# Kernel tuning notes

Measured on AMD Instinct MI355X. Metric: run time of the kernel, lower is better.

Reference implementation:

```python
import jax, jax.numpy as jnp
import numpy as np

DIM = 4096
CAP = 8192
EPS = 1e-8  # torch F.cosine_similarity denominator clamp


def setup_inputs() -> dict:
    key = jax.random.key(0)
    k1, k2, k3, k4, k5, k6 = jax.random.split(key, 6)
    return {
        "query": jax.random.normal(k1, (DIM,), dtype=jnp.float32),
        "memory_bank": jax.random.normal(k2, (CAP, DIM), dtype=jnp.float32),
        "importance": jax.random.uniform(k3, (CAP,), dtype=jnp.float32),
        "age": jax.random.uniform(k4, (CAP,), dtype=jnp.float32) * 1000.0,
        "W_dec": jax.random.normal(k5, (DIM, DIM), dtype=jnp.float32) * (1.0 / np.sqrt(DIM)),
        "b_dec": jax.random.normal(k6, (DIM,), dtype=jnp.float32) * 0.01,
        "top_k": 8,
    }


def reference(query, memory_bank, importance, age, W_dec, b_dec, top_k):
    # Cosine similarity of query against every memory row (torch semantics:
    # dot / max(||q||*||m||, eps)).
    dots = memory_bank @ query                       # [CAP]
    qn = jnp.sqrt(jnp.sum(query * query))
    mn = jnp.sqrt(jnp.sum(memory_bank * memory_bank, axis=1))
    sim = dots / jnp.maximum(qn * mn, EPS)
    # Time-decayed importance weighting.
    weighted = sim * importance * jnp.exp(-0.001 * age)
    # Top-k retrieval, mean-pool retrieved rows, decode.
    _, idx = jax.lax.top_k(weighted, top_k)          # [k]
    retrieved = jnp.mean(memory_bank[idx], axis=0)   # [DIM]
    return retrieved @ W_dec.T + b_dec
```

## Files before the change

### kernel.cpp

```cpp
#include <hip/hip_runtime.h>
#include <math.h>

#define DIM 4096
#define CAP 8192
#define EPS 1e-8f

__global__ __launch_bounds__(256) void score_kernel(
    const float* __restrict__ q,
    const float* __restrict__ mb,
    const float* __restrict__ imp,
    const float* __restrict__ age,
    float* __restrict__ weighted)
{
    const int wave = threadIdx.x >> 6;
    const int lane = threadIdx.x & 63;
    const int row  = (blockIdx.x << 2) + wave;

    const float4* __restrict__ mrow = (const float4*)(mb + (size_t)row * DIM);
    const float4* __restrict__ q4   = (const float4*)q;

    float dot = 0.f, msq = 0.f, qsq = 0.f;
    #pragma unroll 4
    for (int i = lane; i < DIM / 4; i += 64) {
        float4 m  = mrow[i];
        float4 qq = q4[i];
        dot = fmaf(m.w, qq.w, fmaf(m.z, qq.z, fmaf(m.y, qq.y, fmaf(m.x, qq.x, dot))));
        msq = fmaf(m.w, m.w,  fmaf(m.z, m.z,  fmaf(m.y, m.y,  fmaf(m.x, m.x,  msq))));
        qsq = fmaf(qq.w, qq.w, fmaf(qq.z, qq.z, fmaf(qq.y, qq.y, fmaf(qq.x, qq.x, qsq))));
    }
    #pragma unroll
    for (int off = 32; off > 0; off >>= 1) {
        dot += __shfl_down(dot, off, 64);
        msq += __shfl_down(msq, off, 64);
        qsq += __shfl_down(qsq, off, 64);
    }
    if (lane == 0) {
        float denom = fmaxf(sqrtf(qsq) * sqrtf(msq), EPS);
        weighted[row] = (dot / denom) * imp[row] * expf(-0.001f * age[row]);
    }
}

__global__ __launch_bounds__(256) void topk_decode_kernel(
    const float* __restrict__ weighted,
    const float* __restrict__ mb,
    const int* __restrict__ topk_ptr,
    const float* __restrict__ W,
    const float* __restrict__ b,
    float* __restrict__ out)
{
    __shared__ float rbar[DIM];
    __shared__ float rv[4];
    __shared__ int   ri[4];
    __shared__ int   sidx[64];

    const int tid  = threadIdx.x;
    const int wave = tid >> 6;
    const int lane = tid & 63;

    int k = *topk_ptr;
    if (k < 1) k = 1;
    if (k > 64) k = 64;

    const float4* __restrict__ w4 = (const float4*)weighted;
    float4 val[8];
    #pragma unroll
    for (int j = 0; j < 8; ++j) val[j] = w4[(j << 8) + tid];

    float bv = -INFINITY; int bi = 0x7fffffff;
    #pragma unroll
    for (int j = 0; j < 8; ++j) {
        const int base = (j << 10) + (tid << 2);
        if (val[j].x > bv) { bv = val[j].x; bi = base + 0; }
        if (val[j].y > bv) { bv = val[j].y; bi = base + 1; }
        if (val[j].z > bv) { bv = val[j].z; bi = base + 2; }
        if (val[j].w > bv) { bv = val[j].w; bi = base + 3; }
    }

    for (int it = 0; it < k; ++it) {
        float cv = bv; int ci = bi;
        #pragma unroll
        for (int off = 32; off > 0; off >>= 1) {
            float ov = __shfl_down(cv, off, 64);
            int   oi = __shfl_down(ci, off, 64);
            if (ov > cv || (ov == cv && oi < ci)) { cv = ov; ci = oi; }
        }
        if (lane == 0) { rv[wave] = cv; ri[wave] = ci; }
        __syncthreads();
        if (tid == 0) {
            float best = rv[0]; int besti = ri[0];
            #pragma unroll
            for (int w = 1; w < 4; ++w) {
                if (rv[w] > best || (rv[w] == best && ri[w] < besti)) {
                    best = rv[w]; besti = ri[w];
                }
            }
            sidx[it] = besti;
        }
        __syncthreads();
        const int gbi = sidx[it];
        if (((gbi >> 2) & 255) == tid) {
            const int jr = gbi >> 10;
            const int cr = gbi & 3;
            #pragma unroll
            for (int j = 0; j < 8; ++j) {
                if (j == jr) {
                    if (cr == 0) val[j].x = -INFINITY;
                    if (cr == 1) val[j].y = -INFINITY;
                    if (cr == 2) val[j].z = -INFINITY;
                    if (cr == 3) val[j].w = -INFINITY;
                }
            }
            bv = -INFINITY; bi = 0x7fffffff;
            #pragma unroll
            for (int j = 0; j < 8; ++j) {
                const int base = (j << 10) + (tid << 2);
                if (val[j].x > bv) { bv = val[j].x; bi = base + 0; }
                if (val[j].y > bv) { bv = val[j].y; bi = base + 1; }
                if (val[j].z > bv) { bv = val[j].z; bi = base + 2; }
                if (val[j].w > bv) { bv = val[j].w; bi = base + 3; }
            }
        }
    }
    __syncthreads();

    const float inv_k = 1.0f / (float)k;
    float4* __restrict__ rbar4 = (float4*)rbar;
    for (int i = tid; i < DIM / 4; i += 256) {
        float4 acc = make_float4(0.f, 0.f, 0.f, 0.f);
        for (int r = 0; r < k; ++r) {
            const float4 v = ((const float4*)(mb + (size_t)sidx[r] * DIM))[i];
            acc.x += v.x; acc.y += v.y; acc.z += v.z; acc.w += v.w;
        }
        acc.x *= inv_k; acc.y *= inv_k; acc.z *= inv_k; acc.w *= inv_k;
        rbar4[i] = acc;
    }
    __syncthreads();

    const int j = (blockIdx.x << 2) + wave;
    const float4* __restrict__ wrow = (const float4*)(W + (size_t)j * DIM);

    float acc = 0.f;
    #pragma unroll 4
    for (int i = lane; i < DIM / 4; i += 64) {
        float4 w = wrow[i];
        float4 v = rbar4[i];
        acc = fmaf(w.w, v.w, fmaf(w.z, v.z, fmaf(w.y, v.y, fmaf(w.x, v.x, acc))));
    }
    #pragma unroll
    for (int off = 32; off > 0; off >>= 1) acc += __shfl_down(acc, off, 64);
    if (lane == 0) out[j] = acc + b[j];
}

extern "C" void kernel_launch(void* const* d_in, const int* in_sizes, int n_in,
                              void* d_out, int out_size, void* d_ws, size_t ws_size,
                              hipStream_t stream) {
    const float* query      = (const float*)d_in[0];
    const float* memory     = (const float*)d_in[1];
    const float* importance = (const float*)d_in[2];
    const float* age        = (const float*)d_in[3];
    const float* W_dec      = (const float*)d_in[4];
    const float* b_dec      = (const float*)d_in[5];
    const int*   top_k      = (const int*)d_in[6];

    float* weighted = (float*)d_ws;
    float* out      = (float*)d_out;

    score_kernel<<<CAP / 4, 256, 0, stream>>>(query, memory, importance, age, weighted);
    topk_decode_kernel<<<DIM / 4, 256, 0, stream>>>(weighted, memory, top_k,
                                                    W_dec, b_dec, out);
}
```

Before: 254.7 us.

## Make top-k selection wave-local with LDS scores and prefetch W row early

Each wave now runs the full top-k selection on its own, from a copy of all weighted scores staged in shared memory. Selected entries are tracked with per-lane bitmasks, and the lane that owned a winner rescans its candidates. This removes the two block-wide barriers per top-k iteration. The W_dec row is loaded into registers before the selection starts so its global latency overlaps the serial selection, and the gather of the mean-pooled row is split across waves. In exchange, every wave repeats the selection work, and the 64 float4 registers of W plus the 48KB of shared memory per block may reduce occupancy.

```diff
diff --git a/kernel.cpp b/kernel.cpp
--- a/kernel.cpp
+++ b/kernel.cpp
@@ -48,10 +48,9 @@
     const float* __restrict__ b,
     float* __restrict__ out)
 {
+    __shared__ float wv[CAP];
     __shared__ float rbar[DIM];
-    __shared__ float rv[4];
-    __shared__ int   ri[4];
-    __shared__ int   sidx[64];
+    __shared__ int   sidx[4][64];
 
     const int tid  = threadIdx.x;
     const int wave = tid >> 6;
@@ -61,89 +60,85 @@
     if (k < 1) k = 1;
     if (k > 64) k = 64;
 
-    const float4* __restrict__ w4 = (const float4*)weighted;
-    float4 val[8];
+    {
+        const float4* __restrict__ w4  = (const float4*)weighted;
+        float4* __restrict__       wv4 = (float4*)wv;
+        #pragma unroll
+        for (int i = tid; i < CAP / 4; i += 256) wv4[i] = w4[i];
+    }
+    __syncthreads();
+
+    const int j = (blockIdx.x << 2) + wave;
+    const float4* __restrict__ wrow4 = (const float4*)(W + (size_t)j * DIM);
+    float4 wreg[16];
     #pragma unroll
-    for (int j = 0; j < 8; ++j) val[j] = w4[(j << 8) + tid];
+    for (int t = 0; t < 16; ++t) wreg[t] = wrow4[lane + (t << 6)];
 
-    float bv = -INFINITY; int bi = 0x7fffffff;
-    #pragma unroll
-    for (int j = 0; j < 8; ++j) {
-        const int base = (j << 10) + (tid << 2);
-        if (val[j].x > bv) { bv = val[j].x; bi = base + 0; }
-        if (val[j].y > bv) { bv = val[j].y; bi = base + 1; }
-        if (val[j].z > bv) { bv = val[j].z; bi = base + 2; }
-        if (val[j].w > bv) { bv = val[j].w; bi = base + 3; }
-    }
+    const float4* __restrict__ wv4 = (const float4*)wv;
+    unsigned long long cons0 = 0ULL, cons1 = 0ULL;
+
+    float bv; int bi;
+    auto rescan = [&]() {
+        bv = -INFINITY; bi = 0x7fffffff;
+        #pragma unroll
+        for (int t = 0; t < 32; ++t) {
+            const float4 v = wv4[lane + (t << 6)];
+            const int base = (lane << 2) + (t << 8);
+            const unsigned long long m = (t < 16) ? cons0 : cons1;
+            const int sh = (t & 15) << 2;
+            if (!((m >> (sh + 0)) & 1ULL) && v.x > bv) { bv = v.x; bi = base + 0; }
+            if (!((m >> (sh + 1)) & 1ULL) && v.y > bv) { bv = v.y; bi = base + 1; }
+            if (!((m >> (sh + 2)) & 1ULL) && v.z > bv) { bv = v.z; bi = base + 2; }
+            if (!((m >> (sh + 3)) & 1ULL) && v.w > bv) { bv = v.w; bi = base + 3; }
+        }
+    };
+    rescan();
 
     for (int it = 0; it < k; ++it) {
         float cv = bv; int ci = bi;
         #pragma unroll
         for (int off = 32; off > 0; off >>= 1) {
-            float ov = __shfl_down(cv, off, 64);
-            int   oi = __shfl_down(ci, off, 64);
+            float ov = __shfl_xor(cv, off, 64);
+            int   oi = __shfl_xor(ci, off, 64);
             if (ov > cv || (ov == cv && oi < ci)) { cv = ov; ci = oi; }
         }
-        if (lane == 0) { rv[wave] = cv; ri[wave] = ci; }
-        __syncthreads();
-        if (tid == 0) {
-            float best = rv[0]; int besti = ri[0];
-            #pragma unroll
-            for (int w = 1; w < 4; ++w) {
-                if (rv[w] > best || (rv[w] == best && ri[w] < besti)) {
-                    best = rv[w]; besti = ri[w];
-                }
-            }
-            sidx[it] = besti;
+        if (lane == 0) sidx[wave][it] = ci;
+        if (((ci >> 2) & 63) == lane) {
+            const int jp = ((ci >> 8) << 2) | (ci & 3);
+            if (jp < 64) cons0 |= 1ULL << jp;
+            else         cons1 |= 1ULL << (jp - 64);
+            rescan();
         }
-        __syncthreads();
-        const int gbi = sidx[it];
-        if (((gbi >> 2) & 255) == tid) {
-            const int jr = gbi >> 10;
-            const int cr = gbi & 3;
-            #pragma unroll
-            for (int j = 0; j < 8; ++j) {
-                if (j == jr) {
-                    if (cr == 0) val[j].x = -INFINITY;
-                    if (cr == 1) val[j].y = -INFINITY;
-                    if (cr == 2) val[j].z = -INFINITY;
-                    if (cr == 3) val[j].w = -INFINITY;
-                }
-            }
-            bv = -INFINITY; bi = 0x7fffffff;
-            #pragma unroll
-            for (int j = 0; j < 8; ++j) {
-                const int base = (j << 10) + (tid << 2);
-                if (val[j].x > bv) { bv = val[j].x; bi = base + 0; }
-                if (val[j].y > bv) { bv = val[j].y; bi = base + 1; }
-                if (val[j].z > bv) { bv = val[j].z; bi = base + 2; }
-                if (val[j].w > bv) { bv = val[j].w; bi = base + 3; }
-            }
+    }
+    __builtin_amdgcn_wave_barrier();
+
+    float4 racc[4];
+    #pragma unroll
+    for (int t = 0; t < 4; ++t) racc[t] = make_float4(0.f, 0.f, 0.f, 0.f);
+    for (int r = 0; r < k; ++r) {
+        const int idx = sidx[wave][r];
+        const float4* __restrict__ mrow4 = (const float4*)(mb + (size_t)idx * DIM);
+        #pragma unroll
+        for (int t = 0; t < 4; ++t) {
+            const float4 v = mrow4[(wave << 8) + (t << 6) + lane];
+            racc[t].x += v.x; racc[t].y += v.y; racc[t].z += v.z; racc[t].w += v.w;
         }
+    }
+    const float inv_k = 1.0f / (float)k;
+    float4* __restrict__ rbar4 = (float4*)rbar;
+    #pragma unroll
+    for (int t = 0; t < 4; ++t) {
+        racc[t].x *= inv_k; racc[t].y *= inv_k;
+        racc[t].z *= inv_k; racc[t].w *= inv_k;
+        rbar4[(wave << 8) + (t << 6) + lane] = racc[t];
     }
     __syncthreads();
 
-    const float inv_k = 1.0f / (float)k;
-    float4* __restrict__ rbar4 = (float4*)rbar;
-    for (int i = tid; i < DIM / 4; i += 256) {
-        float4 acc = make_float4(0.f, 0.f, 0.f, 0.f);
-        for (int r = 0; r < k; ++r) {
-            const float4 v = ((const float4*)(mb + (size_t)sidx[r] * DIM))[i];
-            acc.x += v.x; acc.y += v.y; acc.z += v.z; acc.w += v.w;
-        }
-        acc.x *= inv_k; acc.y *= inv_k; acc.z *= inv_k; acc.w *= inv_k;
-        rbar4[i] = acc;
-    }
-    __syncthreads();
-
-    const int j = (blockIdx.x << 2) + wave;
-    const float4* __restrict__ wrow = (const float4*)(W + (size_t)j * DIM);
-
     float acc = 0.f;
-    #pragma unroll 4
-    for (int i = lane; i < DIM / 4; i += 64) {
-        float4 w = wrow[i];
-        float4 v = rbar4[i];
+    #pragma unroll
+    for (int t = 0; t < 16; ++t) {
+        const float4 w = wreg[t];
+        const float4 v = rbar4[lane + (t << 6)];
         acc = fmaf(w.w, v.w, fmaf(w.z, v.z, fmaf(w.y, v.y, fmaf(w.x, v.x, acc))));
     }
     #pragma unroll
```

Result: slower. 378.7 us (+48.7%).
